# Kernel optimization log

Measured on AMD Instinct MI355X. Metric: run time of the kernel, lower is better.

## Reference

```python
import jax, jax.numpy as jnp
import numpy as np

B, H, W, DIN = 512, 14, 14, 512
EDIM, K = 64, 256
GRID = 2  # code grid -> code_seq_len = 4


def setup_inputs() -> dict:
    key = jax.random.key(0)
    ks = jax.random.split(key, 12)
    def lin(k, fin, fout):
        return jax.random.normal(k, (fin, fout), jnp.float32) / np.sqrt(fin).astype(np.float32)
    return {
        "features_t0": jax.random.normal(ks[0], (B, H, W, DIN), jnp.float32),
        "features_t1": jax.random.normal(ks[1], (B, H, W, DIN), jnp.float32),
        "enc_w1": lin(ks[2], DIN, 2 * EDIM), "enc_b1": jnp.zeros((2 * EDIM,), jnp.float32),
        "enc_w2": lin(ks[3], 2 * EDIM, EDIM), "enc_b2": jnp.zeros((EDIM,), jnp.float32),
        "dec_w1": lin(ks[4], EDIM, 2 * EDIM), "dec_b1": jnp.zeros((2 * EDIM,), jnp.float32),
        "dec_w2": lin(ks[5], 2 * EDIM, DIN), "dec_b2": jnp.zeros((DIN,), jnp.float32),
        "codebook": jax.random.normal(ks[6], (K, EDIM), jnp.float32),
    }


def reference(features_t0, features_t1, enc_w1, enc_b1, enc_w2, enc_b2,
              dec_w1, dec_b1, dec_w2, dec_b2, codebook):
    # eval-mode forward (no EMA update / data init)
    delta = features_t1 - features_t0                       # [B,H,W,DIN]
    h = jax.nn.gelu(delta @ enc_w1 + enc_b1, approximate=False)
    e = h @ enc_w2 + enc_b2                                 # [B,H,W,EDIM]
    # AdaptiveAvgPool2d((2,2)) on 14x14 == exact 7x7 block mean
    bh, bw = H // GRID, W // GRID
    pooled = e.reshape(B, GRID, bh, GRID, bw, EDIM).mean(axis=(2, 4))  # [B,2,2,EDIM]
    enc = pooled.reshape(B, GRID * GRID, EDIM)              # [B,4,EDIM]

    flat = enc.reshape(-1, EDIM)                            # [B*4, EDIM]
    d2 = ((flat ** 2).sum(-1, keepdims=True)
          - 2.0 * flat @ codebook.T
          + (codebook ** 2).sum(-1))                        # [N,K]
    idx = jnp.argmin(d2, axis=1)                            # [N]
    quantized = codebook[idx]                               # [N,EDIM]

    commitment_loss = jnp.mean((jax.lax.stop_gradient(quantized) - flat) ** 2)
    q_st = flat + jax.lax.stop_gradient(quantized - flat)   # straight-through

    n_tok = flat.shape[0]
    avg_probs = jnp.zeros((K,), flat.dtype).at[idx].add(1.0) / n_tok
    perplexity = jnp.exp(-jnp.sum(avg_probs * jnp.log(avg_probs + 1e-10)))

    q = q_st.reshape(B, GRID * GRID, EDIM)
    hd = jax.nn.gelu(q @ dec_w1 + dec_b1, approximate=False)
    dec = hd @ dec_w2 + dec_b2                              # [B,4,DIN]
    sp = dec.reshape(B, GRID, GRID, DIN).transpose(0, 3, 1, 2)  # [B,DIN,2,2]
    # bilinear, align_corners=False (half-pixel centers, matches jax.image.resize)
    up = jax.image.resize(sp, (B, DIN, H, W), method="bilinear")
    decoded = up.transpose(0, 2, 3, 1)                      # [B,H,W,DIN]

    indices = idx.reshape(B, GRID * GRID)
    return decoded, perplexity, commitment_loss, indices
```

## Files before the change

### kernel.cpp

```cpp
#include <hip/hip_runtime.h>
#include <math.h>

#define N_TOKENS   2048
#define DECODED_SZ 51380224

typedef __attribute__((ext_vector_type(8)))  short bf16x8;
typedef __attribute__((ext_vector_type(16))) float f32x16;
typedef __attribute__((ext_vector_type(4)))  unsigned int u32x4;

__device__ __forceinline__ float gelu_exact(float x) {
    return 0.5f * x * (1.0f + erff(x * 0.70710678118654752440f));
}

__device__ __forceinline__ unsigned int f2bf(float x) {
    unsigned int u = __float_as_uint(x);
    return (u + 0x7fffu + ((u >> 16) & 1u)) >> 16;
}
__device__ __forceinline__ float bf2f(unsigned int b) {
    return __uint_as_float(b << 16);
}

__device__ __forceinline__ unsigned int cvt_pk_bf16(float a, float b) {
    unsigned int p;
    asm("v_cvt_pk_bf16_f32 %0, %1, %2" : "=v"(p) : "v"(a), "v"(b));
    return p;
}
__device__ __forceinline__ void split_pair(float a, float b,
                                           unsigned int& hi, unsigned int& lo) {
    hi = cvt_pk_bf16(a, b);
    const float ra = a - __uint_as_float(hi << 16);
    const float rb = b - __uint_as_float(hi & 0xffff0000u);
    lo = cvt_pk_bf16(ra, rb);
}

union UF { u32x4 u; bf16x8 v; };

__global__ __launch_bounds__(256) void k0_prep_w1(
    const float* __restrict__ w1,
    unsigned short* __restrict__ bth, unsigned short* __restrict__ btl)
{
    const int i  = blockIdx.x * 256 + threadIdx.x;
    const int n  = i >> 6;
    const int kg = i & 63;
    const int k0i = kg * 8;

    unsigned int h[8], lo[8];
#pragma unroll
    for (int j = 0; j < 8; ++j) {
        float v = w1[(k0i + j) * 128 + n];
        h[j]  = f2bf(v);
        lo[j] = f2bf(v - bf2f(h[j]));
    }
    const int idx = (k0i >> 5) * 4096 + n * 32 + (k0i & 31);
    uint4 hv, lv;
    hv.x = h[0]  | (h[1] << 16);  hv.y = h[2]  | (h[3] << 16);
    hv.z = h[4]  | (h[5] << 16);  hv.w = h[6]  | (h[7] << 16);
    lv.x = lo[0] | (lo[1] << 16); lv.y = lo[2] | (lo[3] << 16);
    lv.z = lo[4] | (lo[5] << 16); lv.w = lo[6] | (lo[7] << 16);
    *reinterpret_cast<uint4*>(bth + idx) = hv;
    *reinterpret_cast<uint4*>(btl + idx) = lv;
}

__global__ __launch_bounds__(256, 2) void k1_enc_pool(
    const float* __restrict__ t0, const float* __restrict__ t1,
    const unsigned short* __restrict__ bth, const unsigned short* __restrict__ btl,
    const float* __restrict__ b1,
    float* __restrict__ pooled)
{
    __shared__ float sR[2 * 4 * 128];

    const int t = threadIdx.x;
    const int b = blockIdx.x;
    const int l     = t & 63;
    const int w     = t >> 6;
    const int wm    = w >> 1;
    const int wn    = w & 1;
    const int lan31 = l & 31;
    const int h     = l >> 5;

    const float4* __restrict__ t0v = reinterpret_cast<const float4*>(t0);
    const float4* __restrict__ t1v = reinterpret_cast<const float4*>(t1);

    f32x16 acc[4][2] = {};

    int gbase[4];
    int valid[4];
#pragma unroll
    for (int mi = 0; mi < 4; ++mi) {
        const int row = (wm * 4 + mi) * 32 + lan31;
        valid[mi] = (row < 196);
        gbase[mi] = (b * 196 + (row < 196 ? row : 0)) * 128 + h * 2;
    }
    int boff[2][2];
#pragma unroll
    for (int ni = 0; ni < 2; ++ni) {
        const int col = (wn * 2 + ni) * 32 + lan31;
#pragma unroll
        for (int ks = 0; ks < 2; ++ks)
            boff[ni][ks] = col * 32 + ks * 16 + h * 8;
    }

#pragma unroll 1
    for (int kc = 0; kc < 16; ++kc) {
        bf16x8 bh[2][2], bl[2][2];
#pragma unroll
        for (int ni = 0; ni < 2; ++ni)
#pragma unroll
            for (int ks = 0; ks < 2; ++ks) {
                bh[ni][ks] = *reinterpret_cast<const bf16x8*>(
                    bth + kc * 4096 + boff[ni][ks]);
                bl[ni][ks] = *reinterpret_cast<const bf16x8*>(
                    btl + kc * 4096 + boff[ni][ks]);
            }

#pragma unroll
        for (int mi = 0; mi < 4; ++mi) {
            const int mt = wm * 4 + mi;
            if (mt < 7) {
#pragma unroll
                for (int ks = 0; ks < 2; ++ks) {
                    float d0, d1, d2, d3, d4, d5, d6, d7;
                    if (valid[mi]) {
                        const int g = gbase[mi] + kc * 8 + ks * 4;
                        const float4 x0 = t1v[g],     y0 = t0v[g];
                        const float4 x1 = t1v[g + 1], y1 = t0v[g + 1];
                        d0 = x0.x - y0.x; d1 = x0.y - y0.y;
                        d2 = x0.z - y0.z; d3 = x0.w - y0.w;
                        d4 = x1.x - y1.x; d5 = x1.y - y1.y;
                        d6 = x1.z - y1.z; d7 = x1.w - y1.w;
                    } else {
                        d0 = d1 = d2 = d3 = d4 = d5 = d6 = d7 = 0.0f;
                    }
                    UF ah, al;
                    {
                        unsigned int hw, lw;
                        split_pair(d0, d1, hw, lw); ah.u[0] = hw; al.u[0] = lw;
                        split_pair(d2, d3, hw, lw); ah.u[1] = hw; al.u[1] = lw;
                        split_pair(d4, d5, hw, lw); ah.u[2] = hw; al.u[2] = lw;
                        split_pair(d6, d7, hw, lw); ah.u[3] = hw; al.u[3] = lw;
                    }
#pragma unroll
                    for (int ni = 0; ni < 2; ++ni) {
                        acc[mi][ni] = __builtin_amdgcn_mfma_f32_32x32x16_bf16(
                            ah.v, bh[ni][ks], acc[mi][ni], 0, 0, 0);
                        acc[mi][ni] = __builtin_amdgcn_mfma_f32_32x32x16_bf16(
                            ah.v, bl[ni][ks], acc[mi][ni], 0, 0, 0);
                        acc[mi][ni] = __builtin_amdgcn_mfma_f32_32x32x16_bf16(
                            al.v, bh[ni][ks], acc[mi][ni], 0, 0, 0);
                    }
                }
            }
        }
    }

    float tokacc[2][4] = {};
#pragma unroll
    for (int ni = 0; ni < 2; ++ni) {
        const int col = (wn * 2 + ni) * 32 + lan31;
        const float bias = b1[col];
#pragma unroll
        for (int mi = 0; mi < 4; ++mi) {
#pragma unroll
            for (int reg = 0; reg < 16; ++reg) {
                const int row = (wm * 4 + mi) * 32 + (reg & 3) + 8 * (reg >> 2) + 4 * h;
                if (row < 196) {
                    const float v = gelu_exact(acc[mi][ni][reg] + bias);
                    const int py = row / 14, px = row % 14;
                    const int tok = ((py >= 7) ? 2 : 0) + ((px >= 7) ? 1 : 0);
                    tokacc[ni][tok] += v;
                }
            }
        }
    }
#pragma unroll
    for (int ni = 0; ni < 2; ++ni)
#pragma unroll
        for (int tok = 0; tok < 4; ++tok)
            tokacc[ni][tok] += __shfl_xor(tokacc[ni][tok], 32);
    if (h == 0) {
#pragma unroll
        for (int ni = 0; ni < 2; ++ni)
#pragma unroll
            for (int tok = 0; tok < 4; ++tok)
                sR[(wm * 4 + tok) * 128 + wn * 64 + ni * 32 + lan31] = tokacc[ni][tok];
    }
    __syncthreads();
    for (int i = t; i < 512; i += 256) {
        const int tok = i >> 7, col = i & 127;
        pooled[(b * 4 + tok) * 128 + col] =
            (sR[tok * 128 + col] + sR[(4 + tok) * 128 + col]) * (1.0f / 49.0f);
    }
}

__global__ __launch_bounds__(256, 2) void k2_mid(
    const float* __restrict__ pooled,
    const float* __restrict__ w2,  const float* __restrict__ b2,
    const float* __restrict__ cb,
    const float* __restrict__ dw1, const float* __restrict__ db1,
    const float* __restrict__ dw2, const float* __restrict__ db2,
    float* __restrict__ dec, float* __restrict__ hist, float* __restrict__ commit,
    float* __restrict__ out_idx)
{
    __shared__ float sCB[256 * 66];
    __shared__ float ph[4 * 128];
    __shared__ float es[4 * 64];
    __shared__ float hd[4 * 128];
    __shared__ float rd[256];
    __shared__ int   ri[256];
    __shared__ int   idxs[4];
    __shared__ float dms[4];

    const int t   = threadIdx.x;
    const int tk0 = blockIdx.x * 4;

    if (t < 128)
        reinterpret_cast<float4*>(ph)[t] =
            reinterpret_cast<const float4*>(pooled + tk0 * 128)[t];
    for (int i = t; i < 16384; i += 256) {
        int row = i >> 6, k = i & 63;
        sCB[row * 66 + k] = cb[i];
    }
    __syncthreads();

    {
        const int j = t & 63, tok = t >> 6;
        float a = b2[j];
        const float* phr = ph + tok * 128;
#pragma unroll 8
        for (int k = 0; k < 128; ++k)
            a = fmaf(phr[k], w2[k * 64 + j], a);
        es[tok * 64 + j] = a;
    }
    __syncthreads();

    {
        const int tok = t >> 6, c8 = t & 63;
        float2 ev[32];
#pragma unroll
        for (int k = 0; k < 32; ++k)
            ev[k] = *reinterpret_cast<const float2*>(es + tok * 64 + 2 * k);
        float dmin = 3.4e38f; int imin = 0;
#pragma unroll
        for (int cc = 0; cc < 4; ++cc) {
            const int c = c8 + cc * 64;
            const float* cr = sCB + c * 66;
            float d = 0.f;
#pragma unroll
            for (int k = 0; k < 32; ++k) {
                float2 c2 = *reinterpret_cast<const float2*>(cr + 2 * k);
                float d0 = ev[k].x - c2.x;
                float d1 = ev[k].y - c2.y;
                d = fmaf(d0, d0, d);
                d = fmaf(d1, d1, d);
            }
            if (d < dmin || (d == dmin && c < imin)) { dmin = d; imin = c; }
        }
        rd[t] = dmin; ri[t] = imin;
    }
    __syncthreads();
    for (int s = 32; s > 0; s >>= 1) {
        if ((t & 63) < s) {
            float dn = rd[t + s]; int in = ri[t + s];
            if (dn < rd[t] || (dn == rd[t] && in < ri[t])) { rd[t] = dn; ri[t] = in; }
        }
        __syncthreads();
    }
    if ((t & 63) == 0) {
        const int tok = t >> 6;
        idxs[tok] = ri[t];
        dms[tok]  = rd[t];
        out_idx[tk0 + tok] = (float)ri[t];
        atomicAdd(&hist[ri[t]], 1.0f);
    }
    __syncthreads();
    if (t == 0) {
        float s = dms[0] + dms[1] + dms[2] + dms[3];
        atomicAdd(commit, s);
    }

    {
        const int j = t & 127, half = t >> 7;
        const float bj = db1[j];
        float a0 = bj, a1 = bj;
        const float* q0 = sCB + idxs[half * 2 + 0] * 66;
        const float* q1 = sCB + idxs[half * 2 + 1] * 66;
#pragma unroll 4
        for (int k = 0; k < 64; ++k) {
            const float wv = dw1[k * 128 + j];
            a0 = fmaf(q0[k], wv, a0);
            a1 = fmaf(q1[k], wv, a1);
        }
        hd[(half * 2 + 0) * 128 + j] = gelu_exact(a0);
        hd[(half * 2 + 1) * 128 + j] = gelu_exact(a1);
    }
    __syncthreads();

    {
        float a0[4], a1[4];
        const float bb0 = db2[t], bb1 = db2[t + 256];
#pragma unroll
        for (int q = 0; q < 4; ++q) { a0[q] = bb0; a1[q] = bb1; }
#pragma unroll 2
        for (int j = 0; j < 128; ++j) {
            const float w0 = dw2[j * 512 + t];
            const float w1v = dw2[j * 512 + 256 + t];
#pragma unroll
            for (int q = 0; q < 4; ++q) {
                const float h = hd[q * 128 + j];
                a0[q] = fmaf(h, w0, a0[q]);
                a1[q] = fmaf(h, w1v, a1[q]);
            }
        }
#pragma unroll
        for (int q = 0; q < 4; ++q) {
            dec[(tk0 + q) * 512 + t]       = a0[q];
            dec[(tk0 + q) * 512 + 256 + t] = a1[q];
        }
    }
}

__global__ __launch_bounds__(256) void k2b_final(
    const float* __restrict__ hist, const float* __restrict__ commit,
    float* __restrict__ out2)
{
    __shared__ float red[256];
    const int t = threadIdx.x;
    float p = hist[t] * (1.0f / 2048.0f);
    red[t] = p * logf(p + 1e-10f);
    __syncthreads();
    for (int s = 128; s > 0; s >>= 1) {
        if (t < s) red[t] += red[t + s];
        __syncthreads();
    }
    if (t == 0) {
        out2[0] = expf(-red[0]);
        out2[1] = commit[0] * (1.0f / 131072.0f);
    }
}

__global__ __launch_bounds__(256, 4) void k3_upsample(
    const float* __restrict__ dec, float* __restrict__ out)
{
    __shared__ float  sdec[4 * 512];
    __shared__ float4 wts[196];
    __shared__ int4   offs[196];
    const int b = blockIdx.x, t = threadIdx.x;

    for (int i = t; i < 512; i += 256)
        reinterpret_cast<float4*>(sdec)[i] =
            reinterpret_cast<const float4*>(dec + b * 2048)[i];
    if (t < 196) {
        const int y = t / 14, x = t % 14;
        const float sy = (y + 0.5f) * (1.0f / 7.0f) - 0.5f;
        const float sx = (x + 0.5f) * (1.0f / 7.0f) - 0.5f;
        const int iy = (int)floorf(sy), ix = (int)floorf(sx);
        const float fy = sy - (float)iy, fx = sx - (float)ix;
        const int y0 = min(max(iy, 0), 1), y1 = min(max(iy + 1, 0), 1);
        const int x0 = min(max(ix, 0), 1), x1 = min(max(ix + 1, 0), 1);
        float4 w;
        w.x = (1.f - fy) * (1.f - fx); w.y = (1.f - fy) * fx;
        w.z = fy * (1.f - fx);         w.w = fy * fx;
        wts[t] = w;
        int4 o;
        o.x = (y0 * 2 + x0) * 128; o.y = (y0 * 2 + x1) * 128;
        o.z = (y1 * 2 + x0) * 128; o.w = (y1 * 2 + x1) * 128;
        offs[t] = o;
    }
    __syncthreads();

    const float4* s4 = reinterpret_cast<const float4*>(sdec);
    float4* o4 = reinterpret_cast<float4*>(out) + b * 25088;
    const int c4 = t & 127, ph2 = t >> 7;

#pragma unroll 2
    for (int it = 0; it < 98; ++it) {
        const int pos = ph2 + it * 2;
        const float4 w = wts[pos];
        const int4   o = offs[pos];
        const float4 v00 = s4[o.x + c4];
        const float4 v01 = s4[o.y + c4];
        const float4 v10 = s4[o.z + c4];
        const float4 v11 = s4[o.w + c4];
        float4 r;
        r.x = w.x * v00.x + w.y * v01.x + w.z * v10.x + w.w * v11.x;
        r.y = w.x * v00.y + w.y * v01.y + w.z * v10.y + w.w * v11.y;
        r.z = w.x * v00.z + w.y * v01.z + w.z * v10.z + w.w * v11.z;
        r.w = w.x * v00.w + w.y * v01.w + w.z * v10.w + w.w * v11.w;
        o4[pos * 128 + c4] = r;
    }
}

extern "C" void kernel_launch(void* const* d_in, const int* in_sizes, int n_in,
                              void* d_out, int out_size, void* d_ws, size_t ws_size,
                              hipStream_t stream)
{
    const float* t0  = (const float*)d_in[0];
    const float* t1  = (const float*)d_in[1];
    const float* w1  = (const float*)d_in[2];
    const float* b1  = (const float*)d_in[3];
    const float* w2  = (const float*)d_in[4];
    const float* b2  = (const float*)d_in[5];
    const float* dw1 = (const float*)d_in[6];
    const float* db1 = (const float*)d_in[7];
    const float* dw2 = (const float*)d_in[8];
    const float* db2 = (const float*)d_in[9];
    const float* cb  = (const float*)d_in[10];

    float* out = (float*)d_out;
    float* ws  = (float*)d_ws;

    float* pooled = ws;
    float* dec    = ws + 262144;
    float* hist   = ws + 1310720;
    float* commit = ws + 1310976;

    unsigned short* bth = (unsigned short*)(ws + 262144);
    unsigned short* btl = (unsigned short*)(ws + 262144 + 32768);

    hipMemsetAsync(hist, 0, 257 * sizeof(float), stream);

    k0_prep_w1<<<32, 256, 0, stream>>>(w1, bth, btl);
    k1_enc_pool<<<512, 256, 0, stream>>>(t0, t1, bth, btl, b1, pooled);
    k2_mid<<<512, 256, 0, stream>>>(pooled, w2, b2, cb, dw1, db1, dw2, db2,
                                    dec, hist, commit, out + DECODED_SZ + 2);
    k2b_final<<<1, 256, 0, stream>>>(hist, commit, out + DECODED_SZ);
    k3_upsample<<<512, 256, 0, stream>>>(dec, out);
}
```

Measured before the change: 632.7 us.

## Stage encoder GEMM operands in double-buffered swizzled LDS, split batch over two blocks

The encoder kernel now splits each batch image's 196 rows across two 512-thread blocks. Each block cooperatively loads and splits the delta and W1 tiles into double-buffered, XOR-swizzled shared memory, prefetching the next K chunk during the MFMAs. Previously each wave loaded A and B fragments straight from global memory with scattered per-lane accesses and long serial mi loops. The two blocks' partial pooled sums are written to a larger workspace and combined in k2_mid. This adds one barrier per K step and more shared memory in exchange for coalesced loads and more parallelism.

```diff
diff --git a/kernel.cpp b/kernel.cpp
--- a/kernel.cpp
+++ b/kernel.cpp
@@ -6,7 +6,6 @@
 
 typedef __attribute__((ext_vector_type(8)))  short bf16x8;
 typedef __attribute__((ext_vector_type(16))) float f32x16;
-typedef __attribute__((ext_vector_type(4)))  unsigned int u32x4;
 
 __device__ __forceinline__ float gelu_exact(float x) {
     return 0.5f * x * (1.0f + erff(x * 0.70710678118654752440f));
@@ -33,8 +32,6 @@
     lo = cvt_pk_bf16(ra, rb);
 }
 
-union UF { u32x4 u; bf16x8 v; };
-
 __global__ __launch_bounds__(256) void k0_prep_w1(
     const float* __restrict__ w1,
     unsigned short* __restrict__ bth, unsigned short* __restrict__ btl)
@@ -51,7 +48,8 @@
         h[j]  = f2bf(v);
         lo[j] = f2bf(v - bf2f(h[j]));
     }
-    const int idx = (k0i >> 5) * 4096 + n * 32 + (k0i & 31);
+    const int s   = (k0i & 31) >> 3;
+    const int idx = (k0i >> 5) * 4096 + n * 32 + 8 * (s ^ (n & 3));
     uint4 hv, lv;
     hv.x = h[0]  | (h[1] << 16);  hv.y = h[2]  | (h[3] << 16);
     hv.z = h[4]  | (h[5] << 16);  hv.w = h[6]  | (h[7] << 16);
@@ -61,16 +59,22 @@
     *reinterpret_cast<uint4*>(btl + idx) = lv;
 }
 
-__global__ __launch_bounds__(256, 2) void k1_enc_pool(
+__global__ __launch_bounds__(512, 4) void k1_enc_pool(
     const float* __restrict__ t0, const float* __restrict__ t1,
     const unsigned short* __restrict__ bth, const unsigned short* __restrict__ btl,
     const float* __restrict__ b1,
-    float* __restrict__ pooled)
-{
-    __shared__ float sR[2 * 4 * 128];
-
-    const int t = threadIdx.x;
-    const int b = blockIdx.x;
+    float* __restrict__ part)
+{
+    __shared__ unsigned short sAh[2][4096];
+    __shared__ unsigned short sAl[2][4096];
+    __shared__ unsigned short sBh[2][4096];
+    __shared__ unsigned short sBl[2][4096];
+    __shared__ float sR[4][4][128];
+
+    const int t    = threadIdx.x;
+    const int bid  = blockIdx.x;
+    const int b    = bid >> 1;
+    const int half = bid & 1;
     const int l     = t & 63;
     const int w     = t >> 6;
     const int wm    = w >> 1;
@@ -81,73 +85,90 @@
     const float4* __restrict__ t0v = reinterpret_cast<const float4*>(t0);
     const float4* __restrict__ t1v = reinterpret_cast<const float4*>(t1);
 
-    f32x16 acc[4][2] = {};
-
-    int gbase[4];
-    int valid[4];
-#pragma unroll
-    for (int mi = 0; mi < 4; ++mi) {
-        const int row = (wm * 4 + mi) * 32 + lan31;
-        valid[mi] = (row < 196);
-        gbase[mi] = (b * 196 + (row < 196 ? row : 0)) * 128 + h * 2;
-    }
-    int boff[2][2];
-#pragma unroll
-    for (int ni = 0; ni < 2; ++ni) {
-        const int col = (wn * 2 + ni) * 32 + lan31;
+    int aG[2], aW[2];
+#pragma unroll
+    for (int j = 0; j < 2; ++j) {
+        const int i = t + j * 512;
+        const int r = i >> 3, f = i & 7;
+        const int rg = b * 196 + min(half * 128 + r, 195);
+        aG[j] = rg * 128 + f;
+        aW[j] = r * 32 + 8 * ((f >> 1) ^ (r & 3)) + 4 * (f & 1);
+    }
+    const int bG = t * 8;
+
+    int arOff[2], brOff[2][2];
+    {
+        const int r = wm * 32 + lan31;
 #pragma unroll
         for (int ks = 0; ks < 2; ++ks)
-            boff[ni][ks] = col * 32 + ks * 16 + h * 8;
-    }
-
-#pragma unroll 1
+            arOff[ks] = r * 32 + 8 * ((2 * ks + h) ^ (r & 3));
+#pragma unroll
+        for (int ni = 0; ni < 2; ++ni) {
+            const int c = (wn * 2 + ni) * 32 + lan31;
+#pragma unroll
+            for (int ks = 0; ks < 2; ++ks)
+                brOff[ni][ks] = c * 32 + 8 * ((2 * ks + h) ^ (c & 3));
+        }
+    }
+    const bool tile_ok = (half * 4 + wm) < 7;
+
+    f32x16 acc[2] = {};
+
+    float4 p0a, p0b, p1a, p1b;
+    uint4  qh, ql;
+
+    p1a = t1v[aG[0]]; p0a = t0v[aG[0]];
+    p1b = t1v[aG[1]]; p0b = t0v[aG[1]];
+    qh = *reinterpret_cast<const uint4*>(bth + bG);
+    ql = *reinterpret_cast<const uint4*>(btl + bG);
+
+#pragma unroll 2
     for (int kc = 0; kc < 16; ++kc) {
-        bf16x8 bh[2][2], bl[2][2];
-#pragma unroll
-        for (int ni = 0; ni < 2; ++ni)
+        unsigned short* __restrict__ ah = sAh[kc & 1];
+        unsigned short* __restrict__ al = sAl[kc & 1];
+        unsigned short* __restrict__ bh = sBh[kc & 1];
+        unsigned short* __restrict__ bl = sBl[kc & 1];
+
+        {
+            unsigned int h0, l0, h1, l1;
+            split_pair(p1a.x - p0a.x, p1a.y - p0a.y, h0, l0);
+            split_pair(p1a.z - p0a.z, p1a.w - p0a.w, h1, l1);
+            *reinterpret_cast<uint2*>(ah + aW[0]) = make_uint2(h0, h1);
+            *reinterpret_cast<uint2*>(al + aW[0]) = make_uint2(l0, l1);
+            split_pair(p1b.x - p0b.x, p1b.y - p0b.y, h0, l0);
+            split_pair(p1b.z - p0b.z, p1b.w - p0b.w, h1, l1);
+            *reinterpret_cast<uint2*>(ah + aW[1]) = make_uint2(h0, h1);
+            *reinterpret_cast<uint2*>(al + aW[1]) = make_uint2(l0, l1);
+            *reinterpret_cast<uint4*>(bh + bG) = qh;
+            *reinterpret_cast<uint4*>(bl + bG) = ql;
+        }
+        __syncthreads();
+
+        if (kc < 15) {
+            const int g = (kc + 1) * 8;
+            p1a = t1v[aG[0] + g]; p0a = t0v[aG[0] + g];
+            p1b = t1v[aG[1] + g]; p0b = t0v[aG[1] + g];
+            const int bg2 = (kc + 1) * 4096 + bG;
+            qh = *reinterpret_cast<const uint4*>(bth + bg2);
+            ql = *reinterpret_cast<const uint4*>(btl + bg2);
+        }
+        __builtin_amdgcn_sched_barrier(0);
+
+        if (tile_ok) {
 #pragma unroll
             for (int ks = 0; ks < 2; ++ks) {
-                bh[ni][ks] = *reinterpret_cast<const bf16x8*>(
-                    bth + kc * 4096 + boff[ni][ks]);
-                bl[ni][ks] = *reinterpret_cast<const bf16x8*>(
-                    btl + kc * 4096 + boff[ni][ks]);
-            }
-
-#pragma unroll
-        for (int mi = 0; mi < 4; ++mi) {
-            const int mt = wm * 4 + mi;
-            if (mt < 7) {
-#pragma unroll
-                for (int ks = 0; ks < 2; ++ks) {
-                    float d0, d1, d2, d3, d4, d5, d6, d7;
-                    if (valid[mi]) {
-                        const int g = gbase[mi] + kc * 8 + ks * 4;
-                        const float4 x0 = t1v[g],     y0 = t0v[g];
-                        const float4 x1 = t1v[g + 1], y1 = t0v[g + 1];
-                        d0 = x0.x - y0.x; d1 = x0.y - y0.y;
-                        d2 = x0.z - y0.z; d3 = x0.w - y0.w;
-                        d4 = x1.x - y1.x; d5 = x1.y - y1.y;
-                        d6 = x1.z - y1.z; d7 = x1.w - y1.w;
-                    } else {
-                        d0 = d1 = d2 = d3 = d4 = d5 = d6 = d7 = 0.0f;
-                    }
-                    UF ah, al;
-                    {
-                        unsigned int hw, lw;
-                        split_pair(d0, d1, hw, lw); ah.u[0] = hw; al.u[0] = lw;
-                        split_pair(d2, d3, hw, lw); ah.u[1] = hw; al.u[1] = lw;
-                        split_pair(d4, d5, hw, lw); ah.u[2] = hw; al.u[2] = lw;
-                        split_pair(d6, d7, hw, lw); ah.u[3] = hw; al.u[3] = lw;
-                    }
-#pragma unroll
-                    for (int ni = 0; ni < 2; ++ni) {
-                        acc[mi][ni] = __builtin_amdgcn_mfma_f32_32x32x16_bf16(
-                            ah.v, bh[ni][ks], acc[mi][ni], 0, 0, 0);
-                        acc[mi][ni] = __builtin_amdgcn_mfma_f32_32x32x16_bf16(
-                            ah.v, bl[ni][ks], acc[mi][ni], 0, 0, 0);
-                        acc[mi][ni] = __builtin_amdgcn_mfma_f32_32x32x16_bf16(
-                            al.v, bh[ni][ks], acc[mi][ni], 0, 0, 0);
-                    }
+                const bf16x8 fah = *reinterpret_cast<const bf16x8*>(ah + arOff[ks]);
+                const bf16x8 fal = *reinterpret_cast<const bf16x8*>(al + arOff[ks]);
+#pragma unroll
+                for (int ni = 0; ni < 2; ++ni) {
+                    const bf16x8 fbh = *reinterpret_cast<const bf16x8*>(bh + brOff[ni][ks]);
+                    const bf16x8 fbl = *reinterpret_cast<const bf16x8*>(bl + brOff[ni][ks]);
+                    acc[ni] = __builtin_amdgcn_mfma_f32_32x32x16_bf16(
+                        fah, fbh, acc[ni], 0, 0, 0);
+                    acc[ni] = __builtin_amdgcn_mfma_f32_32x32x16_bf16(
+                        fah, fbl, acc[ni], 0, 0, 0);
+                    acc[ni] = __builtin_amdgcn_mfma_f32_32x32x16_bf16(
+                        fal, fbh, acc[ni], 0, 0, 0);
                 }
             }
         }
@@ -159,16 +180,14 @@
         const int col = (wn * 2 + ni) * 32 + lan31;
         const float bias = b1[col];
 #pragma unroll
-        for (int mi = 0; mi < 4; ++mi) {
-#pragma unroll
-            for (int reg = 0; reg < 16; ++reg) {
-                const int row = (wm * 4 + mi) * 32 + (reg & 3) + 8 * (reg >> 2) + 4 * h;
-                if (row < 196) {
-                    const float v = gelu_exact(acc[mi][ni][reg] + bias);
-                    const int py = row / 14, px = row % 14;
-                    const int tok = ((py >= 7) ? 2 : 0) + ((px >= 7) ? 1 : 0);
-                    tokacc[ni][tok] += v;
-                }
+        for (int reg = 0; reg < 16; ++reg) {
+            const int rl = wm * 32 + (reg & 3) + 8 * (reg >> 2) + 4 * h;
+            const int rg = half * 128 + rl;
+            if (rg < 196) {
+                const float v = gelu_exact(acc[ni][reg] + bias);
+                const int py = rg / 14, px = rg % 14;
+                const int tok = ((py >= 7) ? 2 : 0) + ((px >= 7) ? 1 : 0);
+                tokacc[ni][tok] += v;
             }
         }
     }
@@ -182,18 +201,18 @@
         for (int ni = 0; ni < 2; ++ni)
 #pragma unroll
             for (int tok = 0; tok < 4; ++tok)
-                sR[(wm * 4 + tok) * 128 + wn * 64 + ni * 32 + lan31] = tokacc[ni][tok];
-    }
-    __syncthreads();
-    for (int i = t; i < 512; i += 256) {
-        const int tok = i >> 7, col = i & 127;
-        pooled[(b * 4 + tok) * 128 + col] =
-            (sR[tok * 128 + col] + sR[(4 + tok) * 128 + col]) * (1.0f / 49.0f);
+                sR[wm][tok][wn * 64 + ni * 32 + lan31] = tokacc[ni][tok];
+    }
+    __syncthreads();
+    {
+        const int tok = t >> 7, col = t & 127;
+        part[bid * 512 + tok * 128 + col] =
+            sR[0][tok][col] + sR[1][tok][col] + sR[2][tok][col] + sR[3][tok][col];
     }
 }
 
 __global__ __launch_bounds__(256, 2) void k2_mid(
-    const float* __restrict__ pooled,
+    const float* __restrict__ part,
     const float* __restrict__ w2,  const float* __restrict__ b2,
     const float* __restrict__ cb,
     const float* __restrict__ dw1, const float* __restrict__ db1,
@@ -213,9 +232,18 @@
     const int t   = threadIdx.x;
     const int tk0 = blockIdx.x * 4;
 
-    if (t < 128)
-        reinterpret_cast<float4*>(ph)[t] =
-            reinterpret_cast<const float4*>(pooled + tk0 * 128)[t];
+    if (t < 128) {
+        const float4 x = reinterpret_cast<const float4*>(
+            part + (blockIdx.x * 2 + 0) * 512)[t];
+        const float4 y = reinterpret_cast<const float4*>(
+            part + (blockIdx.x * 2 + 1) * 512)[t];
+        float4 s;
+        s.x = (x.x + y.x) * (1.0f / 49.0f);
+        s.y = (x.y + y.y) * (1.0f / 49.0f);
+        s.z = (x.z + y.z) * (1.0f / 49.0f);
+        s.w = (x.w + y.w) * (1.0f / 49.0f);
+        reinterpret_cast<float4*>(ph)[t] = s;
+    }
     for (int i = t; i < 16384; i += 256) {
         int row = i >> 6, k = i & 63;
         sCB[row * 66 + k] = cb[i];
@@ -409,19 +437,19 @@
     float* out = (float*)d_out;
     float* ws  = (float*)d_ws;
 
-    float* pooled = ws;
-    float* dec    = ws + 262144;
-    float* hist   = ws + 1310720;
-    float* commit = ws + 1310976;
-
-    unsigned short* bth = (unsigned short*)(ws + 262144);
-    unsigned short* btl = (unsigned short*)(ws + 262144 + 32768);
+    float* part   = ws;
+    float* dec    = ws + 524288;
+    float* hist   = ws + 1572864;
+    float* commit = ws + 1573120;
+
+    unsigned short* bth = (unsigned short*)(ws + 524288);
+    unsigned short* btl = (unsigned short*)(ws + 524288 + 32768);
 
     hipMemsetAsync(hist, 0, 257 * sizeof(float), stream);
 
     k0_prep_w1<<<32, 256, 0, stream>>>(w1, bth, btl);
-    k1_enc_pool<<<512, 256, 0, stream>>>(t0, t1, bth, btl, b1, pooled);
-    k2_mid<<<512, 256, 0, stream>>>(pooled, w2, b2, cb, dw1, db1, dw2, db2,
+    k1_enc_pool<<<1024, 512, 0, stream>>>(t0, t1, bth, btl, b1, part);
+    k2_mid<<<512, 256, 0, stream>>>(part, w2, b2, cb, dw1, db1, dw2, db2,
                                     dec, hist, commit, out + DECODED_SZ + 2);
     k2b_final<<<1, 256, 0, stream>>>(hist, commit, out + DECODED_SZ);
     k3_upsample<<<512, 256, 0, stream>>>(dec, out);
```

Measured after the change: 601.4 us. -4.9%, faster.
